# Kernel optimization log

Measured on AMD Instinct MI355X. Metric: run time of the kernel, lower is better.

## Reference

```python
import jax, jax.numpy as jnp
import numpy as np

BETA = 0.25
EPS = 1e-10


def setup_inputs() -> dict:
    key = jax.random.key(0)
    k1, k2 = jax.random.split(key)
    z = jax.random.normal(k1, (32, 256, 32, 32), dtype=jnp.float32)
    # embedding initialized uniform(-1/n_e, 1/n_e) in the torch module
    n_e, e_dim = 1024, 256
    codebook = jax.random.uniform(k2, (n_e, e_dim), dtype=jnp.float32,
                                  minval=-1.0 / n_e, maxval=1.0 / n_e)
    return {"z": z, "codebook": codebook}


def reference(z, codebook):
    # z: (B, C, H, W) with C == e_dim; codebook: (n_e, e_dim)
    n_e = codebook.shape[0]
    zp = jnp.transpose(z, (0, 2, 3, 1))              # (B, H, W, C)
    zf = zp.reshape(-1, zp.shape[-1])                # (N, e_dim)

    # squared euclidean distances: ||z||^2 + ||e||^2 - 2 z.e
    d = (jnp.sum(zf * zf, axis=1, keepdims=True)
         + jnp.sum(codebook * codebook, axis=1)
         - 2.0 * jnp.einsum('nd,kd->nk', zf, codebook))  # (N, n_e)

    min_encoding_indices = jnp.argmin(d, axis=1)     # (N,)
    min_encodings = jax.nn.one_hot(min_encoding_indices, n_e, dtype=zf.dtype)  # (N, n_e)

    # gather quantized vectors (same math as one_hot @ codebook)
    z_q = codebook[min_encoding_indices].reshape(zp.shape)  # (B, H, W, C)

    sg = jax.lax.stop_gradient
    loss = (jnp.mean((sg(z_q) - zp) ** 2)
            + BETA * jnp.mean((z_q - sg(zp)) ** 2))

    # straight-through estimator
    z_q_st = zp + sg(z_q - zp)

    e_mean = jnp.mean(min_encodings, axis=0)         # (n_e,)
    perplexity = jnp.exp(-jnp.sum(e_mean * jnp.log(e_mean + EPS)))

    z_q_out = jnp.transpose(z_q_st, (0, 3, 1, 2))    # (B, C, H, W)
    return (loss, z_q_out, perplexity, min_encodings,
            min_encoding_indices[:, None])
```

## Files before the change

### kernel.cpp

```cpp
#include <hip/hip_runtime.h>
#include <hip/hip_bf16.h>
#include <cstdint>
#include <cstddef>

typedef unsigned short u16;
typedef unsigned char u8;
typedef __attribute__((ext_vector_type(8))) short bf16x8;
typedef __attribute__((ext_vector_type(4))) float f32x4;

#define NPTS 32768
#define NE   1024
#define ED   256
#define ZPLANE 262144

#define OFF_LOSS 0
#define OFF_ZQ   1
#define OFF_PPL  8388609
#define OFF_ENC  8388610
#define OFF_IDX  41943042

#define WS_IDX   0
#define WS_ZZ    131072
#define WS_EE    262144
#define WS_LOSSP 266240
#define NLOSSP   1024
#define WS_HIST  274432
#define WS_ET_FB 331776
#define WS_EH    331776
#define WS_EL    856064
#define WS_ZH    1380352
#define WS_ZL    18157568
#define WS_CCNT  34934784
#define WS_CANDK 35065856
#define WS_CANDS 36638720
#define WS_OCNT  38211584
#define WS_OLIST 38211588
#define WS_NEED  38227972ULL

#define MARGIN 3.0e-4f
#define AMB    2.0e-4f
#define OCAP   4096

__global__ __launch_bounds__(256) void k_prep0(const float* __restrict__ z,
                                               const float* __restrict__ cb,
                                               float* __restrict__ zz,
                                               u16* __restrict__ zh,
                                               u16* __restrict__ zl,
                                               float* __restrict__ ee,
                                               u16* __restrict__ eh,
                                               u16* __restrict__ el,
                                               int* __restrict__ ocnt,
                                               int* __restrict__ hist) {
#pragma clang fp contract(off)
    __shared__ float tile[256 * 33];
    int t = threadIdx.x;
    int blk = blockIdx.x;

    if (blk < 1024) {
        int b   = blk >> 5;
        int hw0 = (blk & 31) * 32;
        const float* zb = z + (size_t)b * ZPLANE + hw0;
        int p4 = (t & 7) * 4, cr = t >> 3;
#pragma unroll
        for (int i = 0; i < 8; ++i) {
            int c = i * 32 + cr;
            float4 v = *(const float4*)(zb + (size_t)c * 1024 + p4);
            float* dst = &tile[c * 33 + p4];
            dst[0] = v.x; dst[1] = v.y; dst[2] = v.z; dst[3] = v.w;
        }
        __syncthreads();
        if (t < 32) {
            int p = t;
            float s[2];
            for (int h = 0; h < 2; ++h) {
                float r[8];
                for (int j = 0; j < 8; ++j) { float v = tile[(h * 128 + j) * 33 + p]; r[j] = v * v; }
                for (int i = 8; i < 128; i += 8)
                    for (int j = 0; j < 8; ++j) { float v = tile[(h * 128 + i + j) * 33 + p]; r[j] += v * v; }
                s[h] = ((r[0] + r[1]) + (r[2] + r[3])) + ((r[4] + r[5]) + (r[6] + r[7]));
            }
            zz[(b << 10) + hw0 + p] = s[0] + s[1];
        }
        int p = t >> 3, cq = t & 7;
        size_t n = (size_t)(b << 10) + hw0 + p;
        u16* dh = zh + n * 256 + cq * 32;
        u16* dl = zl + n * 256 + cq * 32;
#pragma unroll
        for (int g8 = 0; g8 < 4; ++g8) {
            u16 hbuf[8], lbuf[8];
#pragma unroll
            for (int kk = 0; kk < 8; ++kk) {
                float f = tile[(cq * 32 + g8 * 8 + kk) * 33 + p];
                __hip_bfloat16 h = __float2bfloat16(f);
                float hf = __bfloat162float(h);
                __hip_bfloat16 l = __float2bfloat16(f - hf);
                hbuf[kk] = *(u16*)&h; lbuf[kk] = *(u16*)&l;
            }
            *(bf16x8*)(dh + g8 * 8) = *(bf16x8*)&hbuf[0];
            *(bf16x8*)(dl + g8 * 8) = *(bf16x8*)&lbuf[0];
        }
    } else {
        int k = blk - 1024;
        if (k == 0) {
            if (t == 0) *ocnt = 0;
            for (int i = t; i < NE; i += 256) hist[i] = 0;
        }
        float f = cb[(size_t)k * ED + t];
        tile[t] = f;
        __hip_bfloat16 h = __float2bfloat16(f);
        float hf = __bfloat162float(h);
        __hip_bfloat16 l = __float2bfloat16(f - hf);
        eh[(size_t)k * ED + t] = *(u16*)&h;
        el[(size_t)k * ED + t] = *(u16*)&l;
        __syncthreads();
        if (t == 0) {
            float s[2];
            for (int h2 = 0; h2 < 2; ++h2) {
                const float* a = &tile[h2 * 128];
                float r[8];
                for (int j = 0; j < 8; ++j) { float v = a[j]; r[j] = v * v; }
                for (int i = 8; i < 128; i += 8)
                    for (int j = 0; j < 8; ++j) { float v = a[i + j]; r[j] += v * v; }
                s[h2] = ((r[0] + r[1]) + (r[2] + r[3])) + ((r[4] + r[5]) + (r[6] + r[7]));
            }
            ee[k] = s[0] + s[1];
        }
    }
}

__global__ __launch_bounds__(256) void k_prep_old(const float* __restrict__ cb,
                                                  float* __restrict__ ee,
                                                  float* __restrict__ eT,
                                                  int* __restrict__ hist) {
#pragma clang fp contract(off)
    if (blockIdx.x == 0) for (int i = threadIdx.x; i < NE; i += 256) hist[i] = 0;
    int k = blockIdx.x * 256 + threadIdx.x;
    if (k >= NE) return;
    const float* row = cb + (size_t)k * ED;
    float s[2];
    for (int h = 0; h < 2; ++h) {
        const float* a = row + h * 128;
        float r[8];
        for (int j = 0; j < 8; ++j) { float v = a[j]; r[j] = v * v; }
        for (int i = 8; i < 128; i += 8)
            for (int j = 0; j < 8; ++j) { float v = a[i + j]; r[j] += v * v; }
        s[h] = ((r[0] + r[1]) + (r[2] + r[3])) + ((r[4] + r[5]) + (r[6] + r[7]));
    }
    ee[k] = s[0] + s[1];
    for (int c = 0; c < ED; ++c) eT[(size_t)c * NE + k] = row[c];
}

__global__ __launch_bounds__(256) void k_zz(const float* __restrict__ z,
                                            float* __restrict__ zz) {
#pragma clang fp contract(off)
    int n = blockIdx.x * 256 + threadIdx.x;
    int b = n >> 10, hw = n & 1023;
    const float* a0 = z + (size_t)b * ZPLANE + hw;
    float s[2];
    for (int h = 0; h < 2; ++h) {
        const float* a = a0 + (size_t)h * 128 * 1024;
        float r[8];
        for (int j = 0; j < 8; ++j) { float v = a[(size_t)j * 1024]; r[j] = v * v; }
        for (int i = 8; i < 128; i += 8)
            for (int j = 0; j < 8; ++j) { float v = a[(size_t)(i + j) * 1024]; r[j] += v * v; }
        s[h] = ((r[0] + r[1]) + (r[2] + r[3])) + ((r[4] + r[5]) + (r[6] + r[7]));
    }
    zz[n] = s[0] + s[1];
}

__global__ __launch_bounds__(256, 2) void k_filter(const u16* __restrict__ zh,
                                                   const u16* __restrict__ zl,
                                                   const u16* __restrict__ eh,
                                                   const u16* __restrict__ el,
                                                   const float* __restrict__ ee,
                                                   u8* __restrict__ candcnt,
                                                   int* __restrict__ candk,
                                                   float* __restrict__ cands,
                                                   int* __restrict__ ocnt,
                                                   int* __restrict__ olist) {
    __shared__ u16  Bh0[128 * 64];
    __shared__ u16  Bl0[128 * 64];
    __shared__ u16  Bh1[128 * 64];
    __shared__ u16  Bl1[128 * 64];
    __shared__ float eeL[256];
    __shared__ int  cntL[128];
    __shared__ int  ckL[128][3];
    __shared__ float csL[128][3];

    int t = threadIdx.x;
    int lane = t & 63, w = t >> 6;
    int g = blockIdx.x & 255;
    int q = blockIdx.x >> 8;
    int n0 = g * 128;
    int kqbase = q * 256;
    int prow = w * 32 + (lane & 15);
    const u16* zh0 = zh + (size_t)(n0 + prow) * 256;
    const u16* zl0 = zl + (size_t)(n0 + prow) * 256;
    const u16* zh1 = zh0 + 16 * 256;
    const u16* zl1 = zl0 + 16 * 256;
    int koff_lane = (lane >> 4) * 8;

    if (t < 128) cntL[t] = 0;
    eeL[t] = ee[kqbase + t];

    f32x4 acc[2][2][8];
#pragma unroll
    for (int nc = 0; nc < 2; ++nc)
#pragma unroll
        for (int gg = 0; gg < 2; ++gg)
#pragma unroll
            for (int nf = 0; nf < 8; ++nf)
                acc[nc][gg][nf] = (f32x4){0.f, 0.f, 0.f, 0.f};

    for (int kb = 0; kb < 4; ++kb) {
        __syncthreads();
#pragma unroll
        for (int nc = 0; nc < 2; ++nc) {
            int kcbase = kqbase + nc * 128;
            u16* BhX = nc ? Bh1 : Bh0;
            u16* BlX = nc ? Bl1 : Bl0;
#pragma unroll
            for (int i = 0; i < 8; ++i) {
                int f = i * 256 + t;
                int a = f >> 10, r = (f >> 3) & 127, seg = f & 7;
                const u16* src = (a ? el : eh) + (size_t)(kcbase + r) * 256 + kb * 64 + seg * 8;
                bf16x8 v = *(const bf16x8*)src;
                int bo = (r * 128 + seg * 16) ^ ((r & 7) << 4);
                *(bf16x8*)((char*)(a ? BlX : BhX) + bo) = v;
            }
        }
        __syncthreads();
#pragma unroll
        for (int ks2 = 0; ks2 < 2; ++ks2) {
            int ko = kb * 64 + ks2 * 32 + koff_lane;
            bf16x8 ah0 = *(const bf16x8*)(zh0 + ko);
            bf16x8 al0 = *(const bf16x8*)(zl0 + ko);
            bf16x8 ah1 = *(const bf16x8*)(zh1 + ko);
            bf16x8 al1 = *(const bf16x8*)(zl1 + ko);
#pragma unroll
            for (int nf = 0; nf < 8; ++nf) {
                int r = nf * 16 + (lane & 15);
                int bo = (r * 128 + ks2 * 64 + (lane >> 4) * 16) ^ ((r & 7) << 4);
                bf16x8 bh0v = *(const bf16x8*)((const char*)Bh0 + bo);
                bf16x8 bl0v = *(const bf16x8*)((const char*)Bl0 + bo);
                bf16x8 bh1v = *(const bf16x8*)((const char*)Bh1 + bo);
                bf16x8 bl1v = *(const bf16x8*)((const char*)Bl1 + bo);
                acc[0][0][nf] = __builtin_amdgcn_mfma_f32_16x16x32_bf16(ah0, bh0v, acc[0][0][nf], 0, 0, 0);
                acc[0][0][nf] = __builtin_amdgcn_mfma_f32_16x16x32_bf16(al0, bh0v, acc[0][0][nf], 0, 0, 0);
                acc[0][0][nf] = __builtin_amdgcn_mfma_f32_16x16x32_bf16(ah0, bl0v, acc[0][0][nf], 0, 0, 0);
                acc[0][1][nf] = __builtin_amdgcn_mfma_f32_16x16x32_bf16(ah1, bh0v, acc[0][1][nf], 0, 0, 0);
                acc[0][1][nf] = __builtin_amdgcn_mfma_f32_16x16x32_bf16(al1, bh0v, acc[0][1][nf], 0, 0, 0);
                acc[0][1][nf] = __builtin_amdgcn_mfma_f32_16x16x32_bf16(ah1, bl0v, acc[0][1][nf], 0, 0, 0);
                acc[1][0][nf] = __builtin_amdgcn_mfma_f32_16x16x32_bf16(ah0, bh1v, acc[1][0][nf], 0, 0, 0);
                acc[1][0][nf] = __builtin_amdgcn_mfma_f32_16x16x32_bf16(al0, bh1v, acc[1][0][nf], 0, 0, 0);
                acc[1][0][nf] = __builtin_amdgcn_mfma_f32_16x16x32_bf16(ah0, bl1v, acc[1][0][nf], 0, 0, 0);
                acc[1][1][nf] = __builtin_amdgcn_mfma_f32_16x16x32_bf16(ah1, bh1v, acc[1][1][nf], 0, 0, 0);
                acc[1][1][nf] = __builtin_amdgcn_mfma_f32_16x16x32_bf16(al1, bh1v, acc[1][1][nf], 0, 0, 0);
                acc[1][1][nf] = __builtin_amdgcn_mfma_f32_16x16x32_bf16(ah1, bl1v, acc[1][1][nf], 0, 0, 0);
            }
        }
    }
    __syncthreads();

    float runmin[2][4];
#pragma unroll
    for (int gg = 0; gg < 2; ++gg)
#pragma unroll
        for (int j = 0; j < 4; ++j) runmin[gg][j] = 3.4e38f;

#pragma unroll
    for (int nc = 0; nc < 2; ++nc) {
        int kcbase = kqbase + nc * 128;
#pragma unroll
        for (int gg = 0; gg < 2; ++gg) {
#pragma unroll
            for (int nf = 0; nf < 8; ++nf) {
                float eev = eeL[nc * 128 + nf * 16 + (lane & 15)];
                f32x4 d = acc[nc][gg][nf];
                f32x4 s;
#pragma unroll
                for (int j = 0; j < 4; ++j) s[j] = fmaf(-2.f, d[j], eev);
                acc[nc][gg][nf] = s;
            }
#pragma unroll
            for (int j = 0; j < 4; ++j) {
                float m = 3.4e38f;
#pragma unroll
                for (int nf = 0; nf < 8; ++nf) m = fminf(m, acc[nc][gg][nf][j]);
                m = fminf(m, __shfl_xor(m, 1, 64));
                m = fminf(m, __shfl_xor(m, 2, 64));
                m = fminf(m, __shfl_xor(m, 4, 64));
                m = fminf(m, __shfl_xor(m, 8, 64));
                runmin[gg][j] = fminf(runmin[gg][j], m);
                float th = runmin[gg][j] + MARGIN;
                int ml = w * 32 + gg * 16 + (lane >> 4) * 4 + j;
#pragma unroll
                for (int nf = 0; nf < 8; ++nf) {
                    float sv = acc[nc][gg][nf][j];
                    if (sv <= th) {
                        int pos = atomicAdd(&cntL[ml], 1);
                        if (pos < 3) { ckL[ml][pos] = kcbase + nf * 16 + (lane & 15);
                                       csL[ml][pos] = sv; }
                    }
                }
            }
        }
    }
    __syncthreads();
    if (t < 128) {
        int n = n0 + t;
        int cnt = cntL[t];
        candcnt[(size_t)n * 4 + q] = (u8)(cnt > 255 ? 255 : cnt);
        int* dk = candk + (size_t)n * 12 + q * 3;
        float* ds = cands + (size_t)n * 12 + q * 3;
#pragma unroll
        for (int i = 0; i < 3; ++i) {
            dk[i] = (i < cnt) ? ckL[t][i] : 0;
            ds[i] = (i < cnt) ? csL[t][i] : 3.4e38f;
        }
        if (cnt > 3) {
            int pos = atomicAdd(ocnt, 1);
            if (pos < OCAP) olist[pos] = n;
        }
    }
}

__global__ __launch_bounds__(256) void k_score(const float* __restrict__ z,
                                               const float* __restrict__ cb,
                                               const float* __restrict__ ee,
                                               const float* __restrict__ zz,
                                               const u8* __restrict__ candcnt,
                                               const int* __restrict__ candk,
                                               const float* __restrict__ cands,
                                               const int* __restrict__ ocnt,
                                               const int* __restrict__ olist,
                                               int* __restrict__ idx_out) {
    __shared__ float zL[ED];
    __shared__ float rv[4];
    __shared__ int   ri[4];
    __shared__ int   ambN[128];
    __shared__ float ambTh[128];
    __shared__ int   ambCnt;
    int t = threadIdx.x;
    int w = t >> 6, lane = t & 63;
    if (t == 0) ambCnt = 0;
    __syncthreads();

    if (t < 128) {
        int n = blockIdx.x * 128 + t;
        int packed = ((const int*)candcnt)[n];
        int c0 = packed & 255, c1 = (packed >> 8) & 255,
            c2 = (packed >> 16) & 255, c3 = (packed >> 24) & 255;
        if (!((c0 > 3) | (c1 > 3) | (c2 > 3) | (c3 > 3))) {
            int ks[12]; float ss[12];
            const int*   ck = candk + (size_t)n * 12;
            const float* cs = cands + (size_t)n * 12;
#pragma unroll
            for (int p = 0; p < 3; ++p) {
                *(int4*)&ks[p * 4]   = *(const int4*)(ck + p * 4);
                *(float4*)&ss[p * 4] = *(const float4*)(cs + p * 4);
            }
            float gmin = 3.4e38f;
#pragma unroll
            for (int j = 0; j < 12; ++j) gmin = fminf(gmin, ss[j]);
            float th = gmin + AMB;
            int nsurv = 0;
#pragma unroll
            for (int j = 0; j < 12; ++j) nsurv += (ss[j] <= th) ? 1 : 0;

            if (nsurv == 1) {
                int k = 0;
#pragma unroll
                for (int j = 0; j < 12; ++j) if (ss[j] <= th) k = ks[j];
                idx_out[n] = k;
            } else {
                int pos = atomicAdd(&ambCnt, 1);
                ambN[pos] = n; ambTh[pos] = th;
            }
        }
    }
    __syncthreads();

    int acount = ambCnt;
    for (int e = w; e < acount; e += 4) {
        int n = ambN[e]; float th = ambTh[e];
        int b = n >> 10, hw = n & 1023;
        const float* zp = z + (size_t)b * ZPLANE + hw;
        float z0 = zp[(size_t)(lane * 4 + 0) * 1024];
        float z1 = zp[(size_t)(lane * 4 + 1) * 1024];
        float z2 = zp[(size_t)(lane * 4 + 2) * 1024];
        float z3 = zp[(size_t)(lane * 4 + 3) * 1024];
        float zzv = zz[n];
        const int*   ck = candk + (size_t)n * 12;
        const float* cs = cands + (size_t)n * 12;
        float bd = 3.4e38f; int bk = 1 << 30;
#pragma unroll 1
        for (int j = 0; j < 12; ++j) {
            if (cs[j] > th) continue;
            int k = ck[j];
            float4 ev = *(const float4*)(cb + (size_t)k * ED + lane * 4);
            float p = z0 * ev.x;
            p = fmaf(z1, ev.y, p);
            p = fmaf(z2, ev.z, p);
            p = fmaf(z3, ev.w, p);
            p += __shfl_xor(p, 1);
            p += __shfl_xor(p, 2);
            p += __shfl_xor(p, 4);
            p += __shfl_xor(p, 8);
            p += __shfl_xor(p, 16);
            p += __shfl_xor(p, 32);
            float d = (zzv + ee[k]) - 2.f * p;
            if (d < bd || (d == bd && k < bk)) { bd = d; bk = k; }
        }
        if (lane == 0) idx_out[n] = bk;
    }
    __syncthreads();

    int cnt = *ocnt; if (cnt > OCAP) cnt = OCAP;
    for (int i = blockIdx.x; i < cnt; i += gridDim.x) {
        int n = olist[i];
        int b = n >> 10, hw = n & 1023;
        const float* zp = z + (size_t)b * ZPLANE + hw;
        __syncthreads();
        zL[t] = zp[(size_t)t * 1024];
        __syncthreads();
        float zzv = zz[n];
        int k0 = t, k1 = 256 + t, k2 = 512 + t, k3 = 768 + t;
        const float* e0 = cb + (size_t)k0 * ED;
        const float* e1 = cb + (size_t)k1 * ED;
        const float* e2 = cb + (size_t)k2 * ED;
        const float* e3 = cb + (size_t)k3 * ED;
        float a0 = 0.f, a1 = 0.f, a2 = 0.f, a3 = 0.f;
#pragma unroll 8
        for (int c = 0; c < ED; c += 4) {
            float4 z4 = *(const float4*)&zL[c];
            float4 v0 = *(const float4*)(e0 + c);
            float4 v1 = *(const float4*)(e1 + c);
            float4 v2 = *(const float4*)(e2 + c);
            float4 v3 = *(const float4*)(e3 + c);
            a0 = fmaf(z4.x, v0.x, a0); a0 = fmaf(z4.y, v0.y, a0);
            a0 = fmaf(z4.z, v0.z, a0); a0 = fmaf(z4.w, v0.w, a0);
            a1 = fmaf(z4.x, v1.x, a1); a1 = fmaf(z4.y, v1.y, a1);
            a1 = fmaf(z4.z, v1.z, a1); a1 = fmaf(z4.w, v1.w, a1);
            a2 = fmaf(z4.x, v2.x, a2); a2 = fmaf(z4.y, v2.y, a2);
            a2 = fmaf(z4.z, v2.z, a2); a2 = fmaf(z4.w, v2.w, a2);
            a3 = fmaf(z4.x, v3.x, a3); a3 = fmaf(z4.y, v3.y, a3);
            a3 = fmaf(z4.z, v3.z, a3); a3 = fmaf(z4.w, v3.w, a3);
        }
        float d0 = (zzv + ee[k0]) - 2.f * a0;
        float d1 = (zzv + ee[k1]) - 2.f * a1;
        float d2 = (zzv + ee[k2]) - 2.f * a2;
        float d3 = (zzv + ee[k3]) - 2.f * a3;
        float bd = d0; int bk = k0;
        if (d1 < bd) { bd = d1; bk = k1; }
        if (d2 < bd) { bd = d2; bk = k2; }
        if (d3 < bd) { bd = d3; bk = k3; }
        for (int off = 32; off; off >>= 1) {
            float ov = __shfl_down(bd, off);
            int   oi = __shfl_down(bk, off);
            if (ov < bd || (ov == bd && oi < bk)) { bd = ov; bk = oi; }
        }
        if ((t & 63) == 0) { rv[t >> 6] = bd; ri[t >> 6] = bk; }
        __syncthreads();
        if (t == 0) {
            for (int wv = 1; wv < 4; ++wv)
                if (rv[wv] < bd || (rv[wv] == bd && ri[wv] < bk)) { bd = rv[wv]; bk = ri[wv]; }
            idx_out[n] = bk;
        }
    }
}

#define TM 64
#define TK 128
#define CCH 64
__global__ __launch_bounds__(256) void k_main(const float* __restrict__ z,
                                              const float* __restrict__ eT,
                                              const float* __restrict__ ee,
                                              const float* __restrict__ zz,
                                              int* __restrict__ idx_out) {
    __shared__ float zt[CCH][TM];
    __shared__ float et[CCH][TK];
    __shared__ float redv[TM][16];
    __shared__ int   redi[TM][16];
    __shared__ float bestv[TM];
    __shared__ int   besti[TM];
    __shared__ float zzl[TM];
    int t = threadIdx.x;
    int n0 = blockIdx.x * TM;
    int b = n0 >> 10, hw0 = n0 & 1023;
    const float* zb = z + (size_t)b * ZPLANE + hw0;
    int trow = t >> 4, tcol = t & 15;
    if (t < TM) { bestv[t] = 3.4e38f; besti[t] = 0; zzl[t] = zz[n0 + t]; }
    for (int kt = 0; kt < NE / TK; ++kt) {
        int k0 = kt * TK;
        float acc[4][8];
        for (int i = 0; i < 4; ++i)
            for (int j = 0; j < 8; ++j) acc[i][j] = 0.f;
        for (int cc = 0; cc < ED / CCH; ++cc) {
            __syncthreads();
            {
                int m4 = (t & 15) * 4; int cb0 = t >> 4;
                for (int p = 0; p < 4; ++p) {
                    int cl = p * 16 + cb0;
                    float4 v = *(const float4*)(zb + (size_t)(cc * CCH + cl) * 1024 + m4);
                    *(float4*)&zt[cl][m4] = v;
                }
            }
            {
                int k4 = (t & 31) * 4; int cb0 = t >> 5;
                for (int p = 0; p < 8; ++p) {
                    int cl = p * 8 + cb0;
                    float4 v = *(const float4*)(eT + (size_t)(cc * CCH + cl) * 1024 + k0 + k4);
                    *(float4*)&et[cl][k4] = v;
                }
            }
            __syncthreads();
            for (int c = 0; c < CCH; ++c) {
                float4 zm = *(const float4*)&zt[c][trow * 4];
                float4 e0 = *(const float4*)&et[c][tcol * 8];
                float4 e1 = *(const float4*)&et[c][tcol * 8 + 4];
                float zv[4] = {zm.x, zm.y, zm.z, zm.w};
                float ev[8] = {e0.x, e0.y, e0.z, e0.w, e1.x, e1.y, e1.z, e1.w};
                for (int i = 0; i < 4; ++i)
                    for (int j = 0; j < 8; ++j)
                        acc[i][j] = fmaf(zv[i], ev[j], acc[i][j]);
            }
        }
        for (int i = 0; i < 4; ++i) {
            int m = trow * 4 + i;
            float zv = zzl[m];
            float bv = 3.4e38f; int bi = 0;
            for (int j = 0; j < 8; ++j) {
                int k = k0 + tcol * 8 + j;
                float t1 = zv + ee[k];
                float d  = t1 - 2.0f * acc[i][j];
                if (d < bv) { bv = d; bi = k; }
            }
            redv[m][tcol] = bv; redi[m][tcol] = bi;
        }
        __syncthreads();
        if (t < TM) {
            float bv = bestv[t]; int bi = besti[t];
            for (int tc = 0; tc < 16; ++tc) {
                float v = redv[t][tc]; int ix = redi[t][tc];
                if (v < bv || (v == bv && ix < bi)) { bv = v; bi = ix; }
            }
            bestv[t] = bv; besti[t] = bi;
        }
    }
    __syncthreads();
    if (t < TM) idx_out[n0 + t] = besti[t];
}

__global__ __launch_bounds__(256) void k_out(const float* __restrict__ z,
                                             const float* __restrict__ cb,
                                             const int* __restrict__ idx,
                                             float* __restrict__ out,
                                             double* __restrict__ lossp,
                                             int* __restrict__ hist) {
#pragma clang fp contract(off)
    __shared__ float eL[32 * 257];
    __shared__ int idxL[32];
    __shared__ double wsum[4];
    int t = threadIdx.x;
    int blk = blockIdx.x;

    if (blk < 1024) {
        int b   = blk >> 5;
        int hw0 = (blk & 31) * 32;
        int n0  = (b << 10) + hw0;
        if (t < 32) idxL[t] = idx[n0 + t];
        __syncthreads();
        {
            int w = t >> 6, lane = t & 63;
            for (int rr = 0; rr < 8; ++rr) {
                int r = w * 8 + rr;
                int iv = idxL[r];
                float4 v = *(const float4*)(cb + (size_t)iv * ED + lane * 4);
                float* dst = &eL[r * 257 + lane * 4];
                dst[0] = v.x; dst[1] = v.y; dst[2] = v.z; dst[3] = v.w;
            }
        }
        __syncthreads();
        int p4 = (t & 7) * 4, cr = t >> 3;
        const float* zb = z + (size_t)b * ZPLANE + hw0;
        float* ob = out + OFF_ZQ + (size_t)b * ZPLANE + hw0;
        double lsum = 0.0;
#pragma unroll
        for (int i = 0; i < 8; ++i) {
            int c = i * 32 + cr;
            float4 zv4 = *(const float4*)(zb + (size_t)c * 1024 + p4);
            float4 o;
            float d0 = eL[(p4)     * 257 + c] - zv4.x; o.x = zv4.x + d0;
            float d1 = eL[(p4 + 1) * 257 + c] - zv4.y; o.y = zv4.y + d1;
            float d2 = eL[(p4 + 2) * 257 + c] - zv4.z; o.z = zv4.z + d2;
            float d3 = eL[(p4 + 3) * 257 + c] - zv4.w; o.w = zv4.w + d3;
            *(float4*)(ob + (size_t)c * 1024 + p4) = o;
            lsum += (double)(d0 * d0) + (double)(d1 * d1)
                  + (double)(d2 * d2) + (double)(d3 * d3);
        }
        for (int off = 32; off; off >>= 1) lsum += __shfl_down(lsum, off);
        if ((t & 63) == 0) wsum[t >> 6] = lsum;
        __syncthreads();
        if (t == 0) lossp[blk] = (wsum[0] + wsum[1]) + (wsum[2] + wsum[3]);
    } else {
        int blk2 = blk - 1024;
        if (t < 16) atomicAdd(&hist[idx[blk2 * 16 + t]], 1);
        for (int it = 0; it < 16; ++it) {
            int qq = (blk2 * 16 + it) * 256 + t;
            int row  = qq >> 8;
            int col4 = (qq & 255) * 4;
            int iv = idx[row];
            float4 v;
            v.x = (col4     == iv) ? 1.f : 0.f;
            v.y = (col4 + 1 == iv) ? 1.f : 0.f;
            v.z = (col4 + 2 == iv) ? 1.f : 0.f;
            v.w = (col4 + 3 == iv) ? 1.f : 0.f;
            *(float4*)(out + OFF_ENC + (size_t)qq * 4) = v;
            if ((qq & 255) == 0) out[OFF_IDX + row] = (float)iv;
        }
    }
}

__global__ __launch_bounds__(256) void k_final2(const int* __restrict__ hist,
                                                const double* __restrict__ lossp,
                                                float* __restrict__ out) {
    __shared__ double sh[4];
    int t = threadIdx.x;
    double psum = 0.0;
    for (int k = t; k < NE; k += 256) {
        float em = (float)hist[k] / 32768.0f;
        float term = em * logf(em + 1e-10f);
        psum += (double)term;
    }
    for (int off = 32; off; off >>= 1) psum += __shfl_down(psum, off);
    if ((t & 63) == 0) sh[t >> 6] = psum;
    __syncthreads();
    if (t == 0) {
        double tot = (sh[0] + sh[1]) + (sh[2] + sh[3]);
        out[OFF_PPL] = expf(-(float)tot);
    }
    __syncthreads();
    double ls = 0.0;
    for (int i = t; i < NLOSSP; i += 256) ls += lossp[i];
    for (int off = 32; off; off >>= 1) ls += __shfl_down(ls, off);
    __syncthreads();
    if ((t & 63) == 0) sh[t >> 6] = ls;
    __syncthreads();
    if (t == 0) {
        double m = ((sh[0] + sh[1]) + (sh[2] + sh[3])) / 8388608.0;
        float mf = (float)m;
        out[OFF_LOSS] = mf + 0.25f * mf;
    }
}

extern "C" void kernel_launch(void* const* d_in, const int* in_sizes, int n_in,
                              void* d_out, int out_size, void* d_ws, size_t ws_size,
                              hipStream_t stream) {
    const float* z  = (const float*)d_in[0];
    const float* cb = (const float*)d_in[1];
    float* out = (float*)d_out;
    char* ws = (char*)d_ws;

    int*    idx   = (int*)(ws + WS_IDX);
    float*  zz    = (float*)(ws + WS_ZZ);
    float*  ee    = (float*)(ws + WS_EE);
    double* lossp = (double*)(ws + WS_LOSSP);
    int*    hist  = (int*)(ws + WS_HIST);

    if (ws_size >= WS_NEED) {
        u16* eh = (u16*)(ws + WS_EH);
        u16* el = (u16*)(ws + WS_EL);
        u16* zh = (u16*)(ws + WS_ZH);
        u16* zl = (u16*)(ws + WS_ZL);
        u8*  ccnt  = (u8*)(ws + WS_CCNT);
        int* candk = (int*)(ws + WS_CANDK);
        float* cands = (float*)(ws + WS_CANDS);
        int* ocnt  = (int*)(ws + WS_OCNT);
        int* olist = (int*)(ws + WS_OLIST);

        k_prep0 <<<2048, 256, 0, stream>>>(z, cb, zz, zh, zl, ee, eh, el, ocnt, hist);
        k_filter<<<1024, 256, 0, stream>>>(zh, zl, eh, el, ee, ccnt, candk, cands, ocnt, olist);
        k_score <<<256,  256, 0, stream>>>(z, cb, ee, zz, ccnt, candk, cands, ocnt, olist, idx);
        k_out   <<<3072, 256, 0, stream>>>(z, cb, idx, out, lossp, hist);
    } else {
        float* eT = (float*)(ws + WS_ET_FB);
        k_prep_old<<<4,   256, 0, stream>>>(cb, ee, eT, hist);
        k_zz      <<<128, 256, 0, stream>>>(z, zz);
        k_main    <<<512, 256, 0, stream>>>(z, eT, ee, zz, idx);
        k_out     <<<3072,256, 0, stream>>>(z, cb, idx, out, lossp, hist);
    }
    k_final2<<<1, 256, 0, stream>>>(hist, lossp, out);
}
```

Measured before the change: 219.8 us.

## Double-buffer codebook K-slices in LDS with register prefetch in filter kernel

Replaces the load-sync-compute loop over four 64-wide K blocks with an eight-step pipeline over 32-wide K slices. Two LDS buffers alternate while global loads for the next slices and the z fragments are staged in registers. This hides global-load latency behind the MFMA work and needs one barrier per step instead of two. In exchange it raises register pressure from the prefetch registers (the kernel is launch-bounded at 2 blocks per SM) and changes the LDS swizzle layout.

New measurement: 193.7 us (median of 2 runs). 1.13x faster.

```diff
diff --git a/kernel.cpp b/kernel.cpp
--- a/kernel.cpp
+++ b/kernel.cpp
@@ -168,6 +168,46 @@
     zz[n] = s[0] + s[1];
 }
 
+#define LOAD_SLICE(KSV) { \
+    _Pragma("unroll") \
+    for (int i_ = 0; i_ < 8; ++i_) { \
+        int f_ = i_ * 256 + t; \
+        int arr_ = f_ >> 9, r_ = (f_ >> 2) & 127; \
+        const u16* bp_ = (arr_ & 1) ? el : eh; \
+        gbuf[i_] = *(const bf16x8*)(bp_ + (size_t)(kqbase + (arr_ >> 1) * 128 + r_) * 256 + (KSV) * 32 + (f_ & 3) * 8); \
+    } }
+
+#define WRITE_SLICE(BUFP) { \
+    _Pragma("unroll") \
+    for (int i_ = 0; i_ < 8; ++i_) { \
+        int f_ = i_ * 256 + t; \
+        int arr_ = f_ >> 9, r_ = (f_ >> 2) & 127, sl_ = f_ & 3; \
+        *(bf16x8*)&(BUFP)[arr_ * 4096 + r_ * 32 + (sl_ ^ ((r_ >> 1) & 3)) * 8] = gbuf[i_]; \
+    } }
+
+#define MFMA_KS(BUFP) { \
+    _Pragma("unroll") \
+    for (int nf = 0; nf < 8; ++nf) { \
+        int r = nf * 16 + (lane & 15); \
+        int bo = r * 32 + (((lane >> 4) ^ ((r >> 1) & 3)) * 8); \
+        bf16x8 bh0v = *(const bf16x8*)&(BUFP)[bo]; \
+        bf16x8 bl0v = *(const bf16x8*)&(BUFP)[4096 + bo]; \
+        bf16x8 bh1v = *(const bf16x8*)&(BUFP)[8192 + bo]; \
+        bf16x8 bl1v = *(const bf16x8*)&(BUFP)[12288 + bo]; \
+        acc[0][0][nf] = __builtin_amdgcn_mfma_f32_16x16x32_bf16(ah0c, bh0v, acc[0][0][nf], 0, 0, 0); \
+        acc[0][0][nf] = __builtin_amdgcn_mfma_f32_16x16x32_bf16(al0c, bh0v, acc[0][0][nf], 0, 0, 0); \
+        acc[0][0][nf] = __builtin_amdgcn_mfma_f32_16x16x32_bf16(ah0c, bl0v, acc[0][0][nf], 0, 0, 0); \
+        acc[0][1][nf] = __builtin_amdgcn_mfma_f32_16x16x32_bf16(ah1c, bh0v, acc[0][1][nf], 0, 0, 0); \
+        acc[0][1][nf] = __builtin_amdgcn_mfma_f32_16x16x32_bf16(al1c, bh0v, acc[0][1][nf], 0, 0, 0); \
+        acc[0][1][nf] = __builtin_amdgcn_mfma_f32_16x16x32_bf16(ah1c, bl0v, acc[0][1][nf], 0, 0, 0); \
+        acc[1][0][nf] = __builtin_amdgcn_mfma_f32_16x16x32_bf16(ah0c, bh1v, acc[1][0][nf], 0, 0, 0); \
+        acc[1][0][nf] = __builtin_amdgcn_mfma_f32_16x16x32_bf16(al0c, bh1v, acc[1][0][nf], 0, 0, 0); \
+        acc[1][0][nf] = __builtin_amdgcn_mfma_f32_16x16x32_bf16(ah0c, bl1v, acc[1][0][nf], 0, 0, 0); \
+        acc[1][1][nf] = __builtin_amdgcn_mfma_f32_16x16x32_bf16(ah1c, bh1v, acc[1][1][nf], 0, 0, 0); \
+        acc[1][1][nf] = __builtin_amdgcn_mfma_f32_16x16x32_bf16(al1c, bh1v, acc[1][1][nf], 0, 0, 0); \
+        acc[1][1][nf] = __builtin_amdgcn_mfma_f32_16x16x32_bf16(ah1c, bl1v, acc[1][1][nf], 0, 0, 0); \
+    } }
+
 __global__ __launch_bounds__(256, 2) void k_filter(const u16* __restrict__ zh,
                                                    const u16* __restrict__ zl,
                                                    const u16* __restrict__ eh,
@@ -178,10 +218,8 @@
                                                    float* __restrict__ cands,
                                                    int* __restrict__ ocnt,
                                                    int* __restrict__ olist) {
-    __shared__ u16  Bh0[128 * 64];
-    __shared__ u16  Bl0[128 * 64];
-    __shared__ u16  Bh1[128 * 64];
-    __shared__ u16  Bl1[128 * 64];
+    __shared__ u16 Buf0[4 * 4096];
+    __shared__ u16 Buf1[4 * 4096];
     __shared__ float eeL[256];
     __shared__ int  cntL[128];
     __shared__ int  ckL[128][3];
@@ -189,9 +227,9 @@
 
     int t = threadIdx.x;
     int lane = t & 63, w = t >> 6;
-    int g = blockIdx.x & 255;
-    int q = blockIdx.x >> 8;
-    int n0 = g * 128;
+    int pg = blockIdx.x & 255;
+    int q  = blockIdx.x >> 8;
+    int n0 = pg * 128;
     int kqbase = q * 256;
     int prow = w * 32 + (lane & 15);
     const u16* zh0 = zh + (size_t)(n0 + prow) * 256;
@@ -212,55 +250,33 @@
             for (int nf = 0; nf < 8; ++nf)
                 acc[nc][gg][nf] = (f32x4){0.f, 0.f, 0.f, 0.f};
 
-    for (int kb = 0; kb < 4; ++kb) {
-        __syncthreads();
-#pragma unroll
-        for (int nc = 0; nc < 2; ++nc) {
-            int kcbase = kqbase + nc * 128;
-            u16* BhX = nc ? Bh1 : Bh0;
-            u16* BlX = nc ? Bl1 : Bl0;
-#pragma unroll
-            for (int i = 0; i < 8; ++i) {
-                int f = i * 256 + t;
-                int a = f >> 10, r = (f >> 3) & 127, seg = f & 7;
-                const u16* src = (a ? el : eh) + (size_t)(kcbase + r) * 256 + kb * 64 + seg * 8;
-                bf16x8 v = *(const bf16x8*)src;
-                int bo = (r * 128 + seg * 16) ^ ((r & 7) << 4);
-                *(bf16x8*)((char*)(a ? BlX : BhX) + bo) = v;
-            }
-        }
-        __syncthreads();
-#pragma unroll
-        for (int ks2 = 0; ks2 < 2; ++ks2) {
-            int ko = kb * 64 + ks2 * 32 + koff_lane;
-            bf16x8 ah0 = *(const bf16x8*)(zh0 + ko);
-            bf16x8 al0 = *(const bf16x8*)(zl0 + ko);
-            bf16x8 ah1 = *(const bf16x8*)(zh1 + ko);
-            bf16x8 al1 = *(const bf16x8*)(zl1 + ko);
-#pragma unroll
-            for (int nf = 0; nf < 8; ++nf) {
-                int r = nf * 16 + (lane & 15);
-                int bo = (r * 128 + ks2 * 64 + (lane >> 4) * 16) ^ ((r & 7) << 4);
-                bf16x8 bh0v = *(const bf16x8*)((const char*)Bh0 + bo);
-                bf16x8 bl0v = *(const bf16x8*)((const char*)Bl0 + bo);
-                bf16x8 bh1v = *(const bf16x8*)((const char*)Bh1 + bo);
-                bf16x8 bl1v = *(const bf16x8*)((const char*)Bl1 + bo);
-                acc[0][0][nf] = __builtin_amdgcn_mfma_f32_16x16x32_bf16(ah0, bh0v, acc[0][0][nf], 0, 0, 0);
-                acc[0][0][nf] = __builtin_amdgcn_mfma_f32_16x16x32_bf16(al0, bh0v, acc[0][0][nf], 0, 0, 0);
-                acc[0][0][nf] = __builtin_amdgcn_mfma_f32_16x16x32_bf16(ah0, bl0v, acc[0][0][nf], 0, 0, 0);
-                acc[0][1][nf] = __builtin_amdgcn_mfma_f32_16x16x32_bf16(ah1, bh0v, acc[0][1][nf], 0, 0, 0);
-                acc[0][1][nf] = __builtin_amdgcn_mfma_f32_16x16x32_bf16(al1, bh0v, acc[0][1][nf], 0, 0, 0);
-                acc[0][1][nf] = __builtin_amdgcn_mfma_f32_16x16x32_bf16(ah1, bl0v, acc[0][1][nf], 0, 0, 0);
-                acc[1][0][nf] = __builtin_amdgcn_mfma_f32_16x16x32_bf16(ah0, bh1v, acc[1][0][nf], 0, 0, 0);
-                acc[1][0][nf] = __builtin_amdgcn_mfma_f32_16x16x32_bf16(al0, bh1v, acc[1][0][nf], 0, 0, 0);
-                acc[1][0][nf] = __builtin_amdgcn_mfma_f32_16x16x32_bf16(ah0, bl1v, acc[1][0][nf], 0, 0, 0);
-                acc[1][1][nf] = __builtin_amdgcn_mfma_f32_16x16x32_bf16(ah1, bh1v, acc[1][1][nf], 0, 0, 0);
-                acc[1][1][nf] = __builtin_amdgcn_mfma_f32_16x16x32_bf16(al1, bh1v, acc[1][1][nf], 0, 0, 0);
-                acc[1][1][nf] = __builtin_amdgcn_mfma_f32_16x16x32_bf16(ah1, bl1v, acc[1][1][nf], 0, 0, 0);
-            }
-        }
-    }
-    __syncthreads();
+    bf16x8 gbuf[8];
+    LOAD_SLICE(0);
+    WRITE_SLICE(Buf0);
+    LOAD_SLICE(1);
+    bf16x8 ah0c = *(const bf16x8*)(zh0 + koff_lane);
+    bf16x8 al0c = *(const bf16x8*)(zl0 + koff_lane);
+    bf16x8 ah1c = *(const bf16x8*)(zh1 + koff_lane);
+    bf16x8 al1c = *(const bf16x8*)(zl1 + koff_lane);
+    __syncthreads();
+
+    for (int ks = 0; ks < 8; ++ks) {
+        u16* bufC = (ks & 1) ? Buf1 : Buf0;
+        u16* bufN = (ks & 1) ? Buf0 : Buf1;
+        if (ks < 7) WRITE_SLICE(bufN);
+        if (ks < 6) LOAD_SLICE(ks + 2);
+        bf16x8 ah0n, al0n, ah1n, al1n;
+        if (ks < 7) {
+            int ko = (ks + 1) * 32 + koff_lane;
+            ah0n = *(const bf16x8*)(zh0 + ko);
+            al0n = *(const bf16x8*)(zl0 + ko);
+            ah1n = *(const bf16x8*)(zh1 + ko);
+            al1n = *(const bf16x8*)(zl1 + ko);
+        }
+        MFMA_KS(bufC);
+        if (ks < 7) { ah0c = ah0n; al0c = al0n; ah1c = ah1n; al1c = al1n; }
+        __syncthreads();
+    }
 
     float runmin[2][4];
 #pragma unroll
```
